# Optimization experiments

Hardware: AMD Instinct MI355X
Metric: run time of the kernel (lower is better)

Reference implementation:

```python
import jax, jax.numpy as jnp
import numpy as np

N = 8192        # nodes
NFEAT = 256     # input feature dim
NHID = 64       # per-head hidden dim
NHEADS = 4
NCLASS = 121    # PPI label count
ALPHA = 0.2     # LeakyReLU negative slope
NEG_INF = jnp.float32(-9e15)  # pyGAT's mask fill value


def setup_inputs() -> dict:
    key = jax.random.key(0)
    k = jax.random.split(key, 6)
    x = jax.random.normal(k[0], (N, NFEAT), dtype=jnp.float32)
    adj = (jax.random.uniform(k[1], (N, N)) < 0.01).astype(jnp.float32)
    idx = jnp.arange(N)
    adj = adj.at[idx, idx].set(1.0)
    # per-head first-layer params: W [H, nfeat, nhid], a [H, 2*nhid]
    Ws = jax.random.normal(k[2], (NHEADS, NFEAT, NHID), dtype=jnp.float32) * 0.1
    a_heads = jax.random.normal(k[3], (NHEADS, 2 * NHID), dtype=jnp.float32) * 0.1
    # output attention layer params
    W_out = jax.random.normal(k[4], (NHEADS * NHID, NCLASS), dtype=jnp.float32) * 0.1
    a_out = jax.random.normal(k[5], (2 * NCLASS,), dtype=jnp.float32) * 0.1
    return {"x": x, "adj": adj, "Ws": Ws, "a_heads": a_heads,
            "W_out": W_out, "a_out": a_out}


def _gat_head(x, adj, W, a, concat):
    # Dense GraphAttentionLayer (pyGAT), eval mode (dropout off).
    Wh = x @ W                                   # [N, d]
    d = W.shape[1]
    f_src = Wh @ a[:d]                           # [N]  score contribution of node i
    f_dst = Wh @ a[d:]                           # [N]  score contribution of node j
    e = jax.nn.leaky_relu(f_src[:, None] + f_dst[None, :], ALPHA)  # [N, N]
    e = jnp.where(adj > 0, e, NEG_INF)
    att = jax.nn.softmax(e, axis=-1)             # [N, N]
    h = att @ Wh                                 # [N, d]
    return jax.nn.elu(h) if concat else h


def reference(x, adj, Ws, a_heads, W_out, a_out):
    # first multi-head layer (concat=True, elu), vmapped over heads
    heads = jax.vmap(lambda W, a: _gat_head(x, adj, W, a, True))(Ws, a_heads)  # [H, N, nhid]
    h_cat = jnp.transpose(heads, (1, 0, 2)).reshape(x.shape[0], NHEADS * NHID)  # torch.cat(dim=1)
    # output attention layer (concat=False -> raw aggregation)
    return _gat_head(h_cat, adj, W_out, a_out, False)  # [N, nclass]
```

## Files before the change

kernel.cpp:

```cpp
#include <hip/hip_runtime.h>
#include <math.h>

#define N_NODES 8192
#define NFEAT 256
#define NHID 64
#define NHEADS 4
#define NCLASS 121
#define NCPAD 128
#define CAP 256
#define LRALPHA 0.2f

typedef float f32x4 __attribute__((ext_vector_type(4)));

__device__ __forceinline__ float lrelu(float x) { return x > 0.f ? x : LRALPHA * x; }
__device__ __forceinline__ f32x4 splat4(float v) { f32x4 r = {v, v, v, v}; return r; }

__global__ __launch_bounds__(256) void build_csr(const float* __restrict__ adj,
                                                 int* __restrict__ nbr,
                                                 int* __restrict__ deg) {
    int row = blockIdx.x;
    __shared__ int cnt;
    if (threadIdx.x == 0) cnt = 0;
    __syncthreads();
    const f32x4* arow = (const f32x4*)(adj + (size_t)row * N_NODES);
    for (int j4 = threadIdx.x; j4 < N_NODES / 4; j4 += 256) {
        f32x4 v = __builtin_nontemporal_load(&arow[j4]);
        if (v.x > 0.f) { int s = atomicAdd(&cnt, 1); if (s < CAP) nbr[row * CAP + s] = j4 * 4 + 0; }
        if (v.y > 0.f) { int s = atomicAdd(&cnt, 1); if (s < CAP) nbr[row * CAP + s] = j4 * 4 + 1; }
        if (v.z > 0.f) { int s = atomicAdd(&cnt, 1); if (s < CAP) nbr[row * CAP + s] = j4 * 4 + 2; }
        if (v.w > 0.f) { int s = atomicAdd(&cnt, 1); if (s < CAP) nbr[row * CAP + s] = j4 * 4 + 3; }
    }
    __syncthreads();
    if (threadIdx.x == 0) deg[row] = cnt < CAP ? cnt : CAP;
}

__global__ __launch_bounds__(256) void pad_params(const float* __restrict__ Wout,
                                                  const float* __restrict__ aout,
                                                  float* __restrict__ Wpad,
                                                  float* __restrict__ apad) {
    int idx = blockIdx.x * 256 + threadIdx.x;
    if (idx < 256 * NCPAD) {
        int k = idx >> 7, c = idx & 127;
        Wpad[idx] = (c < NCLASS) ? Wout[k * NCLASS + c] : 0.f;
    }
    if (idx < 256) {
        int c = idx & 127;
        float v = 0.f;
        if (c < NCLASS) v = (idx < 128) ? aout[c] : aout[NCLASS + c];
        apad[idx] = v;
    }
}

__global__ __launch_bounds__(256) void gemm1(const float* __restrict__ x,
                                             const float* __restrict__ Ws,
                                             float* __restrict__ Wh1) {
    int h = blockIdx.y;
    int r0 = blockIdx.x * 64;
    __shared__ float xs[64][260];
    for (int t = threadIdx.x; t < 64 * 64; t += 256) {
        int r = t >> 6, c4 = t & 63;
        *(float4*)&xs[r][c4 * 4] = *(const float4*)(x + (size_t)(r0 + r) * NFEAT + c4 * 4);
    }
    __syncthreads();
    int d = threadIdx.x & 63;
    int rb = (threadIdx.x >> 6) * 16;
    const float* W = Ws + (size_t)h * NFEAT * NHID + d;
    float acc[16] = {};
    for (int k4 = 0; k4 < NFEAT; k4 += 4) {
        float b0 = W[(k4 + 0) * NHID];
        float b1 = W[(k4 + 1) * NHID];
        float b2 = W[(k4 + 2) * NHID];
        float b3 = W[(k4 + 3) * NHID];
#pragma unroll
        for (int r = 0; r < 16; r++) {
            float4 a = *(const float4*)&xs[rb + r][k4];
            acc[r] += a.x * b0 + a.y * b1 + a.z * b2 + a.w * b3;
        }
    }
#pragma unroll
    for (int r = 0; r < 16; r++)
        Wh1[(size_t)(r0 + rb + r) * (NHEADS * NHID) + h * NHID + d] = acc[r];
}

__global__ __launch_bounds__(256) void attn_coef1(const float* __restrict__ Wh1,
                                                  const float* __restrict__ a_heads,
                                                  float* __restrict__ fs1t,
                                                  float* __restrict__ fd1t) {
    int i = blockIdx.x;
    int h = threadIdx.x >> 6, lane = threadIdx.x & 63;
    float wh = Wh1[(size_t)i * (NHEADS * NHID) + h * NHID + lane];
    float s = wh * a_heads[h * 2 * NHID + lane];
    float dd = wh * a_heads[h * 2 * NHID + NHID + lane];
#pragma unroll
    for (int o = 32; o > 0; o >>= 1) { s += __shfl_down(s, o); dd += __shfl_down(dd, o); }
    if (lane == 0) { fs1t[i * 4 + h] = s; fd1t[i * 4 + h] = dd; }
}

__global__ __launch_bounds__(256) void attn_agg1(const int* __restrict__ nbr,
                                                 const int* __restrict__ deg,
                                                 const float* __restrict__ Wh1,
                                                 const float* __restrict__ fs1t,
                                                 const float* __restrict__ fd1t,
                                                 float* __restrict__ hcat) {
    int w = threadIdx.x >> 6, lane = threadIdx.x & 63;
    int i = blockIdx.x * 4 + w;
    __shared__ int nbrs[4][CAP];
    __shared__ float pbuf[4][CAP][4];
    int dg = deg[i];
    for (int t = lane; t < dg; t += 64)
        nbrs[w][t] = nbr[i * CAP + t];
    f32x4 fsi = *(const f32x4*)(fs1t + (size_t)i * 4);
    f32x4 e[4];
    f32x4 m4 = {-3.4e38f, -3.4e38f, -3.4e38f, -3.4e38f};
#pragma unroll
    for (int k = 0; k < 4; k++) {
        int t = lane + (k << 6);
        if (t < dg) {
            int j = nbrs[w][t];
            f32x4 fdj = *(const f32x4*)(fd1t + (size_t)j * 4);
            f32x4 ev;
            ev.x = lrelu(fsi.x + fdj.x);
            ev.y = lrelu(fsi.y + fdj.y);
            ev.z = lrelu(fsi.z + fdj.z);
            ev.w = lrelu(fsi.w + fdj.w);
            e[k] = ev;
            m4.x = fmaxf(m4.x, ev.x); m4.y = fmaxf(m4.y, ev.y);
            m4.z = fmaxf(m4.z, ev.z); m4.w = fmaxf(m4.w, ev.w);
        }
    }
#pragma unroll
    for (int o = 32; o > 0; o >>= 1) {
        m4.x = fmaxf(m4.x, __shfl_xor(m4.x, o));
        m4.y = fmaxf(m4.y, __shfl_xor(m4.y, o));
        m4.z = fmaxf(m4.z, __shfl_xor(m4.z, o));
        m4.w = fmaxf(m4.w, __shfl_xor(m4.w, o));
    }
    f32x4 s4 = {0.f, 0.f, 0.f, 0.f};
#pragma unroll
    for (int k = 0; k < 4; k++) {
        int t = lane + (k << 6);
        if (t < dg) {
            f32x4 p;
            p.x = __expf(e[k].x - m4.x);
            p.y = __expf(e[k].y - m4.y);
            p.z = __expf(e[k].z - m4.z);
            p.w = __expf(e[k].w - m4.w);
            *(f32x4*)&pbuf[w][t][0] = p;
            s4 += p;
        }
    }
#pragma unroll
    for (int o = 32; o > 0; o >>= 1) {
        s4.x += __shfl_xor(s4.x, o);
        s4.y += __shfl_xor(s4.y, o);
        s4.z += __shfl_xor(s4.z, o);
        s4.w += __shfl_xor(s4.w, o);
    }
    __syncthreads();
    int hl = lane >> 4;
    const float* wrow = Wh1 + 4 * lane;
    f32x4 acc = {0.f, 0.f, 0.f, 0.f};
#pragma unroll 4
    for (int t = 0; t < dg; t++) {
        int j = nbrs[w][t];
        float p = pbuf[w][t][hl];
        f32x4 wv = *(const f32x4*)(wrow + (size_t)j * (NHEADS * NHID));
        acc += wv * splat4(p);
    }
    float sh = hl == 0 ? s4.x : hl == 1 ? s4.y : hl == 2 ? s4.z : s4.w;
    acc.x /= sh; acc.y /= sh; acc.z /= sh; acc.w /= sh;
    acc.x = acc.x > 0.f ? acc.x : expm1f(acc.x);
    acc.y = acc.y > 0.f ? acc.y : expm1f(acc.y);
    acc.z = acc.z > 0.f ? acc.z : expm1f(acc.z);
    acc.w = acc.w > 0.f ? acc.w : expm1f(acc.w);
    *(f32x4*)(hcat + (size_t)i * (NHEADS * NHID) + 4 * lane) = acc;
}

__global__ __launch_bounds__(256) void gemm2(const float* __restrict__ hcat,
                                             const float* __restrict__ Wpad,
                                             float* __restrict__ Wh2) {
    int r0 = blockIdx.x * 64;
    __shared__ float xs[64][260];
    for (int t = threadIdx.x; t < 64 * 64; t += 256) {
        int r = t >> 6, c4 = t & 63;
        *(float4*)&xs[r][c4 * 4] = *(const float4*)(hcat + (size_t)(r0 + r) * 256 + c4 * 4);
    }
    __syncthreads();
    int c0 = (threadIdx.x & 63) * 2;
    int rb = (threadIdx.x >> 6) * 16;
    float acc0[16] = {}, acc1[16] = {};
    for (int k4 = 0; k4 < 256; k4 += 4) {
        float2 b0 = *(const float2*)&Wpad[(k4 + 0) * NCPAD + c0];
        float2 b1 = *(const float2*)&Wpad[(k4 + 1) * NCPAD + c0];
        float2 b2 = *(const float2*)&Wpad[(k4 + 2) * NCPAD + c0];
        float2 b3 = *(const float2*)&Wpad[(k4 + 3) * NCPAD + c0];
#pragma unroll
        for (int r = 0; r < 16; r++) {
            float4 a = *(const float4*)&xs[rb + r][k4];
            acc0[r] += a.x * b0.x + a.y * b1.x + a.z * b2.x + a.w * b3.x;
            acc1[r] += a.x * b0.y + a.y * b1.y + a.z * b2.y + a.w * b3.y;
        }
    }
#pragma unroll
    for (int r = 0; r < 16; r++) {
        float2 v = make_float2(acc0[r], acc1[r]);
        *(float2*)&Wh2[(size_t)(r0 + rb + r) * NCPAD + c0] = v;
    }
}

__global__ __launch_bounds__(256) void attn_coef2(const float* __restrict__ Wh2,
                                                  const float* __restrict__ apad,
                                                  float* __restrict__ fs2,
                                                  float* __restrict__ fd2) {
    int i = blockIdx.x * 4 + (threadIdx.x >> 6);
    int lane = threadIdx.x & 63;
    float w0 = Wh2[(size_t)i * NCPAD + lane];
    float w1 = Wh2[(size_t)i * NCPAD + 64 + lane];
    float s = w0 * apad[lane] + w1 * apad[64 + lane];
    float dd = w0 * apad[128 + lane] + w1 * apad[192 + lane];
#pragma unroll
    for (int o = 32; o > 0; o >>= 1) { s += __shfl_down(s, o); dd += __shfl_down(dd, o); }
    if (lane == 0) { fs2[i] = s; fd2[i] = dd; }
}

__global__ __launch_bounds__(256) void attn_agg2(const int* __restrict__ nbr,
                                                 const int* __restrict__ deg,
                                                 const float* __restrict__ Wh2,
                                                 const float* __restrict__ fs2,
                                                 const float* __restrict__ fd2,
                                                 float* __restrict__ out) {
    int w = threadIdx.x >> 6, lane = threadIdx.x & 63;
    int i = blockIdx.x * 4 + w;
    __shared__ int nbrs[4][CAP];
    __shared__ float pbuf[4][CAP];
    int dg = deg[i];
    for (int t = lane; t < dg; t += 64)
        nbrs[w][t] = nbr[i * CAP + t];
    float fsi = fs2[i];
    float e[4];
    float m = -3.4e38f;
#pragma unroll
    for (int k = 0; k < 4; k++) {
        int t = lane + (k << 6);
        if (t < dg) {
            float ev = lrelu(fsi + fd2[nbrs[w][t]]);
            e[k] = ev;
            m = fmaxf(m, ev);
        }
    }
#pragma unroll
    for (int o = 32; o > 0; o >>= 1) m = fmaxf(m, __shfl_xor(m, o));
    float s = 0.f;
#pragma unroll
    for (int k = 0; k < 4; k++) {
        int t = lane + (k << 6);
        if (t < dg) {
            float p = __expf(e[k] - m);
            pbuf[w][t] = p;
            s += p;
        }
    }
#pragma unroll
    for (int o = 32; o > 0; o >>= 1) s += __shfl_xor(s, o);
    __syncthreads();
    int eg = lane >> 5, c = lane & 31;
    const float* wrow = Wh2 + 4 * c;
    f32x4 acc = {0.f, 0.f, 0.f, 0.f};
    for (int tt = 0; tt < dg; tt += 2) {
        int t = tt + eg;
        int tc = t < dg ? t : 0;
        float p = t < dg ? pbuf[w][tc] : 0.f;
        int j = nbrs[w][tc];
        f32x4 wv = *(const f32x4*)(wrow + (size_t)j * NCPAD);
        acc += wv * splat4(p);
    }
    acc.x += __shfl_xor(acc.x, 32);
    acc.y += __shfl_xor(acc.y, 32);
    acc.z += __shfl_xor(acc.z, 32);
    acc.w += __shfl_xor(acc.w, 32);
    if (eg == 0) {
        int c4 = c * 4;
#pragma unroll
        for (int q = 0; q < 4; q++)
            if (c4 + q < NCLASS) out[(size_t)i * NCLASS + c4 + q] = acc[q] / s;
    }
}


extern "C" void kernel_launch(void* const* d_in, const int* in_sizes, int n_in,
                              void* d_out, int out_size, void* d_ws, size_t ws_size,
                              hipStream_t stream) {
    const float* x       = (const float*)d_in[0];
    const float* adj     = (const float*)d_in[1];
    const float* Ws      = (const float*)d_in[2];
    const float* a_heads = (const float*)d_in[3];
    const float* Wout    = (const float*)d_in[4];
    const float* aout    = (const float*)d_in[5];
    float* out = (float*)d_out;

    char* ws = (char*)d_ws;
    size_t off = 0;
    auto alloc = [&](size_t bytes) { void* p = ws + off; off = (off + bytes + 255) & ~(size_t)255; return p; };
    int*   nbr  = (int*)  alloc((size_t)N_NODES * CAP * 4);
    int*   deg  = (int*)  alloc((size_t)N_NODES * 4);
    float* Wh1  = (float*)alloc((size_t)N_NODES * NHEADS * NHID * 4);
    float* fs1t = (float*)alloc((size_t)N_NODES * 4 * 4);
    float* fd1t = (float*)alloc((size_t)N_NODES * 4 * 4);
    float* hcat = (float*)alloc((size_t)N_NODES * NHEADS * NHID * 4);
    float* Wh2  = (float*)alloc((size_t)N_NODES * NCPAD * 4);
    float* fs2  = (float*)alloc((size_t)N_NODES * 4);
    float* fd2  = (float*)alloc((size_t)N_NODES * 4);
    float* Wpad = (float*)alloc((size_t)256 * NCPAD * 4);
    float* apad = (float*)alloc((size_t)256 * 4);

    build_csr<<<N_NODES, 256, 0, stream>>>(adj, nbr, deg);
    pad_params<<<128, 256, 0, stream>>>(Wout, aout, Wpad, apad);
    gemm1<<<dim3(N_NODES / 64, NHEADS), 256, 0, stream>>>(x, Ws, Wh1);
    attn_coef1<<<N_NODES, 256, 0, stream>>>(Wh1, a_heads, fs1t, fd1t);
    attn_agg1<<<N_NODES / 4, 256, 0, stream>>>(nbr, deg, Wh1, fs1t, fd1t, hcat);
    gemm2<<<N_NODES / 64, 256, 0, stream>>>(hcat, Wpad, Wh2);
    attn_coef2<<<N_NODES / 4, 256, 0, stream>>>(Wh2, apad, fs2, fd2);
    attn_agg2<<<N_NODES / 4, 256, 0, stream>>>(nbr, deg, Wh2, fs2, fd2, out);
}
```

Baseline: 485.2 us.

## Fuse attention coefficient reductions into GEMM epilogues and use nontemporal stores

Folds the per-node attention score dot products (f_src/f_dst) into the epilogues of gemm1 and gemm2, using wave shuffles over the accumulators. This removes the two attn_coef kernels, their launches and their re-reads of Wh1/Wh2. It also switches output writes to nontemporal stores and raises unroll factors in both aggregation loops. The risk is that nontemporal stores of Wh1/Wh2 may evict data the following gather kernels want to find in cache.

```diff
diff --git a/kernel.cpp b/kernel.cpp
--- a/kernel.cpp
+++ b/kernel.cpp
@@ -11,6 +11,7 @@
 #define LRALPHA 0.2f
 
 typedef float f32x4 __attribute__((ext_vector_type(4)));
+typedef float f32x2 __attribute__((ext_vector_type(2)));
 
 __device__ __forceinline__ float lrelu(float x) { return x > 0.f ? x : LRALPHA * x; }
 __device__ __forceinline__ f32x4 splat4(float v) { f32x4 r = {v, v, v, v}; return r; }
@@ -53,7 +54,10 @@
 
 __global__ __launch_bounds__(256) void gemm1(const float* __restrict__ x,
                                              const float* __restrict__ Ws,
-                                             float* __restrict__ Wh1) {
+                                             const float* __restrict__ a_heads,
+                                             float* __restrict__ Wh1,
+                                             float* __restrict__ fs1t,
+                                             float* __restrict__ fd1t) {
     int h = blockIdx.y;
     int r0 = blockIdx.x * 64;
     __shared__ float xs[64][260];
@@ -77,23 +81,21 @@
             acc[r] += a.x * b0 + a.y * b1 + a.z * b2 + a.w * b3;
         }
     }
-#pragma unroll
-    for (int r = 0; r < 16; r++)
-        Wh1[(size_t)(r0 + rb + r) * (NHEADS * NHID) + h * NHID + d] = acc[r];
-}
-
-__global__ __launch_bounds__(256) void attn_coef1(const float* __restrict__ Wh1,
-                                                  const float* __restrict__ a_heads,
-                                                  float* __restrict__ fs1t,
-                                                  float* __restrict__ fd1t) {
-    int i = blockIdx.x;
-    int h = threadIdx.x >> 6, lane = threadIdx.x & 63;
-    float wh = Wh1[(size_t)i * (NHEADS * NHID) + h * NHID + lane];
-    float s = wh * a_heads[h * 2 * NHID + lane];
-    float dd = wh * a_heads[h * 2 * NHID + NHID + lane];
-#pragma unroll
-    for (int o = 32; o > 0; o >>= 1) { s += __shfl_down(s, o); dd += __shfl_down(dd, o); }
-    if (lane == 0) { fs1t[i * 4 + h] = s; fd1t[i * 4 + h] = dd; }
+    float ah_s = a_heads[h * 2 * NHID + d];
+    float ah_d = a_heads[h * 2 * NHID + NHID + d];
+#pragma unroll
+    for (int r = 0; r < 16; r++) {
+        __builtin_nontemporal_store(acc[r],
+            &Wh1[(size_t)(r0 + rb + r) * (NHEADS * NHID) + h * NHID + d]);
+        float s = acc[r] * ah_s;
+        float dd = acc[r] * ah_d;
+#pragma unroll
+        for (int o = 32; o > 0; o >>= 1) { s += __shfl_xor(s, o); dd += __shfl_xor(dd, o); }
+        if (d == 0) {
+            __builtin_nontemporal_store(s, &fs1t[(size_t)(r0 + rb + r) * 4 + h]);
+            __builtin_nontemporal_store(dd, &fd1t[(size_t)(r0 + rb + r) * 4 + h]);
+        }
+    }
 }
 
 __global__ __launch_bounds__(256) void attn_agg1(const int* __restrict__ nbr,
@@ -160,7 +162,7 @@
     int hl = lane >> 4;
     const float* wrow = Wh1 + 4 * lane;
     f32x4 acc = {0.f, 0.f, 0.f, 0.f};
-#pragma unroll 4
+#pragma unroll 8
     for (int t = 0; t < dg; t++) {
         int j = nbrs[w][t];
         float p = pbuf[w][t][hl];
@@ -173,12 +175,16 @@
     acc.y = acc.y > 0.f ? acc.y : expm1f(acc.y);
     acc.z = acc.z > 0.f ? acc.z : expm1f(acc.z);
     acc.w = acc.w > 0.f ? acc.w : expm1f(acc.w);
-    *(f32x4*)(hcat + (size_t)i * (NHEADS * NHID) + 4 * lane) = acc;
+    f32x4 r = acc;
+    __builtin_nontemporal_store(r, (f32x4*)(hcat + (size_t)i * (NHEADS * NHID) + 4 * lane));
 }
 
 __global__ __launch_bounds__(256) void gemm2(const float* __restrict__ hcat,
                                              const float* __restrict__ Wpad,
-                                             float* __restrict__ Wh2) {
+                                             const float* __restrict__ apad,
+                                             float* __restrict__ Wh2,
+                                             float* __restrict__ fs2,
+                                             float* __restrict__ fd2) {
     int r0 = blockIdx.x * 64;
     __shared__ float xs[64][260];
     for (int t = threadIdx.x; t < 64 * 64; t += 256) {
@@ -201,26 +207,21 @@
             acc1[r] += a.x * b0.y + a.y * b1.y + a.z * b2.y + a.w * b3.y;
         }
     }
+    float as0 = apad[c0], as1 = apad[c0 + 1];
+    float ad0 = apad[128 + c0], ad1 = apad[128 + c0 + 1];
 #pragma unroll
     for (int r = 0; r < 16; r++) {
-        float2 v = make_float2(acc0[r], acc1[r]);
-        *(float2*)&Wh2[(size_t)(r0 + rb + r) * NCPAD + c0] = v;
-    }
-}
-
-__global__ __launch_bounds__(256) void attn_coef2(const float* __restrict__ Wh2,
-                                                  const float* __restrict__ apad,
-                                                  float* __restrict__ fs2,
-                                                  float* __restrict__ fd2) {
-    int i = blockIdx.x * 4 + (threadIdx.x >> 6);
-    int lane = threadIdx.x & 63;
-    float w0 = Wh2[(size_t)i * NCPAD + lane];
-    float w1 = Wh2[(size_t)i * NCPAD + 64 + lane];
-    float s = w0 * apad[lane] + w1 * apad[64 + lane];
-    float dd = w0 * apad[128 + lane] + w1 * apad[192 + lane];
-#pragma unroll
-    for (int o = 32; o > 0; o >>= 1) { s += __shfl_down(s, o); dd += __shfl_down(dd, o); }
-    if (lane == 0) { fs2[i] = s; fd2[i] = dd; }
+        f32x2 v = {acc0[r], acc1[r]};
+        __builtin_nontemporal_store(v, (f32x2*)&Wh2[(size_t)(r0 + rb + r) * NCPAD + c0]);
+        float s = acc0[r] * as0 + acc1[r] * as1;
+        float dd = acc0[r] * ad0 + acc1[r] * ad1;
+#pragma unroll
+        for (int o = 32; o > 0; o >>= 1) { s += __shfl_xor(s, o); dd += __shfl_xor(dd, o); }
+        if ((threadIdx.x & 63) == 0) {
+            __builtin_nontemporal_store(s, &fs2[r0 + rb + r]);
+            __builtin_nontemporal_store(dd, &fd2[r0 + rb + r]);
+        }
+    }
 }
 
 __global__ __launch_bounds__(256) void attn_agg2(const int* __restrict__ nbr,
@@ -266,6 +267,7 @@
     int eg = lane >> 5, c = lane & 31;
     const float* wrow = Wh2 + 4 * c;
     f32x4 acc = {0.f, 0.f, 0.f, 0.f};
+#pragma unroll 4
     for (int tt = 0; tt < dg; tt += 2) {
         int t = tt + eg;
         int tc = t < dg ? t : 0;
@@ -282,7 +284,8 @@
         int c4 = c * 4;
 #pragma unroll
         for (int q = 0; q < 4; q++)
-            if (c4 + q < NCLASS) out[(size_t)i * NCLASS + c4 + q] = acc[q] / s;
+            if (c4 + q < NCLASS)
+                __builtin_nontemporal_store(acc[q] / s, &out[(size_t)i * NCLASS + c4 + q]);
     }
 }
 
@@ -315,10 +318,8 @@
 
     build_csr<<<N_NODES, 256, 0, stream>>>(adj, nbr, deg);
     pad_params<<<128, 256, 0, stream>>>(Wout, aout, Wpad, apad);
-    gemm1<<<dim3(N_NODES / 64, NHEADS), 256, 0, stream>>>(x, Ws, Wh1);
-    attn_coef1<<<N_NODES, 256, 0, stream>>>(Wh1, a_heads, fs1t, fd1t);
+    gemm1<<<dim3(N_NODES / 64, NHEADS), 256, 0, stream>>>(x, Ws, a_heads, Wh1, fs1t, fd1t);
     attn_agg1<<<N_NODES / 4, 256, 0, stream>>>(nbr, deg, Wh1, fs1t, fd1t, hcat);
-    gemm2<<<N_NODES / 64, 256, 0, stream>>>(hcat, Wpad, Wh2);
-    attn_coef2<<<N_NODES / 4, 256, 0, stream>>>(Wh2, apad, fs2, fd2);
+    gemm2<<<N_NODES / 64, 256, 0, stream>>>(hcat, Wpad, apad, Wh2, fs2, fd2);
     attn_agg2<<<N_NODES / 4, 256, 0, stream>>>(nbr, deg, Wh2, fs2, fd2, out);
 }
```

Result: slower. 509.2 us (+5.0%).
